# Performance work log

Measured on AMD Instinct MI355X. Metric: run time of the kernel, lower is better.

Reference implementation:

```python
import jax, jax.numpy as jnp
import numpy as np

N_NODES = 10000
N_EDGES = 320000
D_IN = 256
D_OUT = 256
NEG_SLOPE = 0.2


def setup_inputs() -> dict:
    key = jax.random.key(0)
    ks = jax.random.split(key, 8)
    feature = jax.random.normal(ks[0], (N_NODES, D_IN), dtype=jnp.float32)
    src = jax.random.randint(ks[1], (N_EDGES,), 0, N_NODES, dtype=jnp.int32)
    dst = jax.random.randint(ks[2], (N_EDGES,), 0, N_NODES, dtype=jnp.int32)
    # Xavier-ish scaled weights
    s = 1.0 / np.sqrt(D_IN)
    W_s = jax.random.normal(ks[3], (D_OUT, D_IN), dtype=jnp.float32) * s
    W_t = jax.random.normal(ks[4], (D_OUT, D_IN), dtype=jnp.float32) * s
    W_attn = jax.random.normal(ks[5], (1, D_OUT), dtype=jnp.float32) * (1.0 / np.sqrt(D_OUT))
    W_fc = jax.random.normal(ks[6], (D_OUT, D_IN), dtype=jnp.float32) * s
    b_fc = jnp.zeros((D_OUT,), dtype=jnp.float32)
    return {"feature": feature, "src": src, "dst": dst,
            "W_s": W_s, "W_t": W_t, "W_attn": W_attn,
            "W_fc": W_fc, "b_fc": b_fc}


def reference(feature, src, dst, W_s, W_t, W_attn, W_fc, b_fc):
    n = feature.shape[0]
    # Project at node level, then gather (same math as projecting gathered feats).
    proj_s = feature @ W_s.T          # [N, D_OUT]
    proj_t = feature @ W_t.T          # [N, D_OUT]
    # Edge attention logits: attn(LeakyReLU(h_dst + h_src))
    z = proj_s[src] + proj_t[dst]     # [E, D_OUT]
    z = jnp.where(z >= 0, z, NEG_SLOPE * z)
    e = (z @ W_attn.T)[:, 0]          # [E]
    # edge_softmax with norm_by='src': softmax over outgoing edges of each src node
    m = jax.ops.segment_max(e, src, num_segments=n)          # [N]
    m = jnp.where(jnp.isfinite(m), m, 0.0)                   # guard empty segments
    e_exp = jnp.exp(e - m[src])                               # [E]
    denom = jax.ops.segment_sum(e_exp, src, num_segments=n)  # [N]
    alpha = e_exp / denom[src]                                # [E]
    # message = src feature * alpha; reduce = sum at dst
    msg = feature[src] * alpha[:, None]                       # [E, D_IN]
    agg = jax.ops.segment_sum(msg, dst, num_segments=n)       # [N, D_IN]
    # final linear
    return agg @ W_fc.T + b_fc
```

## Files before the change

kernel.cpp:

```cpp
#include <hip/hip_runtime.h>
#include <math.h>

#define N_NODES 10000
#define N_EDGES 320000
#define D 256
#define NEG_SLOPE 0.2f
#define BCAP 96
#define BLOCK 256
#define NF4 (N_NODES * D / 4)
#define NW4 (256 * 256 / 4)
#define NTILE_M 157
#define NTILES (NTILE_M * 12)
#define FILL_BLOCKS ((N_EDGES + BLOCK - 1) / BLOCK)

typedef unsigned short ushortT;
typedef __attribute__((ext_vector_type(8))) short bf16x8;
typedef __attribute__((ext_vector_type(4))) float f32x4;

__device__ __forceinline__ unsigned short f2bf(float f) {
  unsigned int u = __float_as_uint(f);
  u += 0x7FFFu + ((u >> 16) & 1u);
  return (unsigned short)(u >> 16);
}
__device__ __forceinline__ float bf2f(unsigned short u) {
  return __uint_as_float((unsigned int)u << 16);
}

__global__ void prep_kernel(const float* __restrict__ feat,
                            const float* __restrict__ Ws,
                            const float* __restrict__ Wt,
                            const float* __restrict__ Wfc,
                            ushortT* __restrict__ featb,
                            ushortT* __restrict__ Wcat,
                            int* __restrict__ cnt,
                            float* __restrict__ denom) {
  const int g = blockIdx.x * blockDim.x + threadIdx.x;
  if (g < NF4) {
    float4 v = ((const float4*)feat)[g];
    ushort4 u;
    u.x = f2bf(v.x); u.y = f2bf(v.y); u.z = f2bf(v.z); u.w = f2bf(v.w);
    ((ushort4*)featb)[g] = u;
    return;
  }
  const int gi = g - NF4;
  if (gi < 3 * NW4) {
    const float* W = (gi < NW4) ? Ws : ((gi < 2 * NW4) ? Wt : Wfc);
    const int off = gi - ((gi < NW4) ? 0 : ((gi < 2 * NW4) ? NW4 : 2 * NW4));
    float4 v = ((const float4*)W)[off];
    ushort4 u;
    u.x = f2bf(v.x); u.y = f2bf(v.y); u.z = f2bf(v.z); u.w = f2bf(v.w);
    ((ushort4*)Wcat)[gi] = u;
    return;
  }
  const int gn = gi - 3 * NW4;
  if (gn < N_NODES) {
    cnt[gn] = 0;
    denom[gn] = 0.f;
  }
}

__global__ __launch_bounds__(256, 2) void proj_fill_kernel(
    const ushortT* __restrict__ featb,
    const ushortT* __restrict__ Wcat,
    const int* __restrict__ src, const int* __restrict__ dst,
    int* __restrict__ cnt, int* __restrict__ src_b,
    ushortT* __restrict__ ps, ushortT* __restrict__ pt,
    ushortT* __restrict__ fcp) {
  if (blockIdx.x >= NTILES) {
    const int i = (blockIdx.x - NTILES) * BLOCK + threadIdx.x;
    if (i < N_EDGES) {
      const int dn = dst[i];
      const int slot = atomicAdd(&cnt[dn], 1);
      if (slot < BCAP) src_b[dn * BCAP + slot] = src[i];
    }
    return;
  }

  const int m0 = (blockIdx.x % NTILE_M) * 64;
  const int by = blockIdx.x / NTILE_M;
  ushortT* outp = (by < 4) ? ps : ((by < 8) ? pt : fcp);
  const int col0 = (by & 3) * 64;
  const int n0 = by * 64;

  const int wave = threadIdx.x >> 6;
  const int lane = threadIdx.x & 63;
  const int quad = lane >> 4;
  const int l16 = lane & 15;

  const int m_base = m0 + (wave & 1) * 32;
  const int wn = wave >> 1;
  const int nb = n0 + wn * 32;

  const bf16x8 zero8 = {0, 0, 0, 0, 0, 0, 0, 0};
  const int r0 = m_base + l16;
  const int r1 = r0 + 16;

  bf16x8 a0r[8], a1r[8];
#pragma unroll
  for (int kk = 0; kk < 8; ++kk) {
    const int ko = kk * 32 + quad * 8;
    a0r[kk] = (r0 < N_NODES) ? *(const bf16x8*)(featb + (size_t)r0 * D + ko) : zero8;
    a1r[kk] = (r1 < N_NODES) ? *(const bf16x8*)(featb + (size_t)r1 * D + ko) : zero8;
  }

  f32x4 acc[2][2];
#pragma unroll
  for (int i = 0; i < 2; ++i)
#pragma unroll
    for (int j = 0; j < 2; ++j) acc[i][j] = (f32x4){0.f, 0.f, 0.f, 0.f};

#pragma unroll
  for (int kk = 0; kk < 8; ++kk) {
    const int ko = kk * 32 + quad * 8;
    bf16x8 b0 = *(const bf16x8*)(Wcat + (size_t)(nb + l16) * D + ko);
    bf16x8 b1 = *(const bf16x8*)(Wcat + (size_t)(nb + 16 + l16) * D + ko);
    acc[0][0] = __builtin_amdgcn_mfma_f32_16x16x32_bf16(a0r[kk], b0, acc[0][0], 0, 0, 0);
    acc[0][1] = __builtin_amdgcn_mfma_f32_16x16x32_bf16(a0r[kk], b1, acc[0][1], 0, 0, 0);
    acc[1][0] = __builtin_amdgcn_mfma_f32_16x16x32_bf16(a1r[kk], b0, acc[1][0], 0, 0, 0);
    acc[1][1] = __builtin_amdgcn_mfma_f32_16x16x32_bf16(a1r[kk], b1, acc[1][1], 0, 0, 0);
  }

#pragma unroll
  for (int mi = 0; mi < 2; ++mi) {
#pragma unroll
    for (int r = 0; r < 4; ++r) {
      const int row = m_base + mi * 16 + quad * 4 + r;
      if (row < N_NODES) {
#pragma unroll
        for (int ni = 0; ni < 2; ++ni) {
          const int col = col0 + wn * 32 + ni * 16 + l16;
          outp[(size_t)row * D + col] = f2bf(acc[mi][ni][r]);
        }
      }
    }
  }
}

__global__ __launch_bounds__(256) void logit_bucket_kernel(
    const ushortT* __restrict__ ps,
    const ushortT* __restrict__ pt,
    const int* __restrict__ cnt,
    const int* __restrict__ src_b,
    const float* __restrict__ Wattn,
    float* __restrict__ expv_b,
    float* __restrict__ denom) {
  const int n = blockIdx.x;
  const int cn = min(cnt[n], BCAP);
  if (cn == 0) return;
  const int wave = threadIdx.x >> 6;
  const int lane = threadIdx.x & 63;
  const int half = lane >> 5;
  const int l32 = lane & 31;
  const int grp = wave * 2 + half;
  const int base = n * BCAP;

  bf16x8 bu = *(const bf16x8*)(pt + (size_t)n * D + l32 * 8);
  float b[8], w[8];
  const float4 w0 = *(const float4*)(Wattn + l32 * 8);
  const float4 w1 = *(const float4*)(Wattn + l32 * 8 + 4);
  w[0] = w0.x; w[1] = w0.y; w[2] = w0.z; w[3] = w0.w;
  w[4] = w1.x; w[5] = w1.y; w[6] = w1.z; w[7] = w1.w;
#pragma unroll
  for (int i = 0; i < 8; ++i) b[i] = bf2f((unsigned short)bu[i]);

  int j = grp;
  for (; j + 24 < cn; j += 32) {
    const int s0 = src_b[base + j];
    const int s1 = src_b[base + j + 8];
    const int s2 = src_b[base + j + 16];
    const int s3 = src_b[base + j + 24];
    bf16x8 au0 = *(const bf16x8*)(ps + (size_t)s0 * D + l32 * 8);
    bf16x8 au1 = *(const bf16x8*)(ps + (size_t)s1 * D + l32 * 8);
    bf16x8 au2 = *(const bf16x8*)(ps + (size_t)s2 * D + l32 * 8);
    bf16x8 au3 = *(const bf16x8*)(ps + (size_t)s3 * D + l32 * 8);
    float sum0 = 0.f, sum1 = 0.f, sum2 = 0.f, sum3 = 0.f;
#pragma unroll
    for (int i = 0; i < 8; ++i) {
      float z0 = bf2f((unsigned short)au0[i]) + b[i];
      float z1 = bf2f((unsigned short)au1[i]) + b[i];
      float z2 = bf2f((unsigned short)au2[i]) + b[i];
      float z3 = bf2f((unsigned short)au3[i]) + b[i];
      z0 = fmaxf(z0, NEG_SLOPE * z0);
      z1 = fmaxf(z1, NEG_SLOPE * z1);
      z2 = fmaxf(z2, NEG_SLOPE * z2);
      z3 = fmaxf(z3, NEG_SLOPE * z3);
      sum0 = fmaf(w[i], z0, sum0);
      sum1 = fmaf(w[i], z1, sum1);
      sum2 = fmaf(w[i], z2, sum2);
      sum3 = fmaf(w[i], z3, sum3);
    }
#pragma unroll
    for (int off = 16; off > 0; off >>= 1) {
      sum0 += __shfl_down(sum0, off, 32);
      sum1 += __shfl_down(sum1, off, 32);
      sum2 += __shfl_down(sum2, off, 32);
      sum3 += __shfl_down(sum3, off, 32);
    }
    if (l32 == 0) {
      float ex0 = __expf(sum0), ex1 = __expf(sum1);
      float ex2 = __expf(sum2), ex3 = __expf(sum3);
      expv_b[base + j] = ex0;
      expv_b[base + j + 8] = ex1;
      expv_b[base + j + 16] = ex2;
      expv_b[base + j + 24] = ex3;
      atomicAdd(&denom[s0], ex0);
      atomicAdd(&denom[s1], ex1);
      atomicAdd(&denom[s2], ex2);
      atomicAdd(&denom[s3], ex3);
    }
  }
  for (; j < cn; j += 8) {
    const int s = src_b[base + j];
    bf16x8 au = *(const bf16x8*)(ps + (size_t)s * D + l32 * 8);
    float sum = 0.f;
#pragma unroll
    for (int i = 0; i < 8; ++i) {
      float z = bf2f((unsigned short)au[i]) + b[i];
      z = fmaxf(z, NEG_SLOPE * z);
      sum = fmaf(w[i], z, sum);
    }
#pragma unroll
    for (int off = 16; off > 0; off >>= 1) sum += __shfl_down(sum, off, 32);
    if (l32 == 0) {
      float ex = __expf(sum);
      expv_b[base + j] = ex;
      atomicAdd(&denom[s], ex);
    }
  }
}

__global__ __launch_bounds__(64) void prescale_kernel(
    const ushortT* __restrict__ fcp,
    const float* __restrict__ denom,
    ushortT* __restrict__ fcpsb) {
  const int n = blockIdx.x;
  const int t = threadIdx.x;
  const float inv = 1.0f / denom[n];
  ushort4 v = ((const ushort4*)(fcp + (size_t)n * D))[t];
  ushort4 o;
  o.x = f2bf(bf2f(v.x) * inv);
  o.y = f2bf(bf2f(v.y) * inv);
  o.z = f2bf(bf2f(v.z) * inv);
  o.w = f2bf(bf2f(v.w) * inv);
  ((ushort4*)(fcpsb + (size_t)n * D))[t] = o;
}

__global__ __launch_bounds__(256) void gather_agg_kernel(
    const ushortT* __restrict__ fcpsb,
    const int* __restrict__ cnt,
    const int* __restrict__ src_b,
    const float* __restrict__ expv_b,
    const float* __restrict__ b_fc,
    float* __restrict__ out) {
  __shared__ float red[8][D];
  const int n = blockIdx.x;
  const int tid = threadIdx.x;
  const int wave = tid >> 6;
  const int lane = tid & 63;
  const int half = lane >> 5;
  const int l32 = lane & 31;
  const int grp = wave * 2 + half;
  const int cn = min(cnt[n], BCAP);
  const int base = n * BCAP;

  float acc[8];
#pragma unroll
  for (int i = 0; i < 8; ++i) acc[i] = 0.f;

  int j = grp;
  for (; j + 24 < cn; j += 32) {
    const int s0 = src_b[base + j];
    const int s1 = src_b[base + j + 8];
    const int s2 = src_b[base + j + 16];
    const int s3 = src_b[base + j + 24];
    const float a0 = expv_b[base + j];
    const float a1 = expv_b[base + j + 8];
    const float a2 = expv_b[base + j + 16];
    const float a3 = expv_b[base + j + 24];
    bf16x8 f0 = *(const bf16x8*)(fcpsb + (size_t)s0 * D + l32 * 8);
    bf16x8 f1 = *(const bf16x8*)(fcpsb + (size_t)s1 * D + l32 * 8);
    bf16x8 f2 = *(const bf16x8*)(fcpsb + (size_t)s2 * D + l32 * 8);
    bf16x8 f3 = *(const bf16x8*)(fcpsb + (size_t)s3 * D + l32 * 8);
#pragma unroll
    for (int i = 0; i < 8; ++i) {
      acc[i] = fmaf(a0, bf2f((unsigned short)f0[i]), acc[i]);
      acc[i] = fmaf(a1, bf2f((unsigned short)f1[i]), acc[i]);
      acc[i] = fmaf(a2, bf2f((unsigned short)f2[i]), acc[i]);
      acc[i] = fmaf(a3, bf2f((unsigned short)f3[i]), acc[i]);
    }
  }
  for (; j < cn; j += 8) {
    const int s = src_b[base + j];
    const float a = expv_b[base + j];
    bf16x8 fu = *(const bf16x8*)(fcpsb + (size_t)s * D + l32 * 8);
#pragma unroll
    for (int i = 0; i < 8; ++i)
      acc[i] = fmaf(a, bf2f((unsigned short)fu[i]), acc[i]);
  }
  *(float4*)&red[grp][l32 * 8] = make_float4(acc[0], acc[1], acc[2], acc[3]);
  *(float4*)&red[grp][l32 * 8 + 4] = make_float4(acc[4], acc[5], acc[6], acc[7]);
  __syncthreads();
  float o = b_fc[tid];
#pragma unroll
  for (int g = 0; g < 8; ++g) o += red[g][tid];
  out[(size_t)n * D + tid] = o;
}

extern "C" void kernel_launch(void* const* d_in, const int* in_sizes, int n_in,
                              void* d_out, int out_size, void* d_ws, size_t ws_size,
                              hipStream_t stream) {
  const float* feat  = (const float*)d_in[0];
  const int*   src   = (const int*)d_in[1];
  const int*   dst   = (const int*)d_in[2];
  const float* Ws    = (const float*)d_in[3];
  const float* Wt    = (const float*)d_in[4];
  const float* Wattn = (const float*)d_in[5];
  const float* Wfc   = (const float*)d_in[6];
  const float* bfc   = (const float*)d_in[7];
  float* out = (float*)d_out;

  ushortT* ps    = (ushortT*)d_ws;
  ushortT* pt    = ps + (size_t)N_NODES * D;
  ushortT* fcp   = pt + (size_t)N_NODES * D;
  ushortT* featb = fcp + (size_t)N_NODES * D;
  ushortT* Wcat  = featb + (size_t)N_NODES * D;
  float* expv_b  = (float*)(Wcat + (size_t)768 * 256);
  float* denom   = expv_b + (size_t)N_NODES * BCAP;
  int*   cnt     = (int*)(denom + N_NODES);
  int*   src_b   = cnt + N_NODES;
  ushortT* fcpsb = featb;

  const int prep_items = NF4 + 3 * NW4 + N_NODES;
  prep_kernel<<<(prep_items + BLOCK - 1) / BLOCK, BLOCK, 0, stream>>>(
      feat, Ws, Wt, Wfc, featb, Wcat, cnt, denom);
  proj_fill_kernel<<<NTILES + FILL_BLOCKS, BLOCK, 0, stream>>>(
      featb, Wcat, src, dst, cnt, src_b, ps, pt, fcp);
  logit_bucket_kernel<<<N_NODES, BLOCK, 0, stream>>>(ps, pt, cnt, src_b, Wattn, expv_b, denom);
  prescale_kernel<<<N_NODES, 64, 0, stream>>>(fcp, denom, fcpsb);
  gather_agg_kernel<<<N_NODES, BLOCK, 0, stream>>>(fcpsb, cnt, src_b, expv_b, bfc, out);
}
```

Baseline: 179.2 us.

## Stage feature tile in LDS, preload weights, reorder fill blocks first

The projection GEMM now loads each 64-row feature tile cooperatively into padded shared memory, with each wave reading its A fragments from LDS and holding the B weight fragments in registers. Tile blocks are ordered so the 12 column tiles for the same rows run next to each other, improving L2 reuse of the feature rows. Edge-fill blocks are moved to the front of the grid, and launch bounds are raised to allow more resident blocks. The cost is added LDS traffic and a block barrier, and the higher occupancy target may put pressure on registers.

```diff
diff --git a/kernel.cpp b/kernel.cpp
--- a/kernel.cpp
+++ b/kernel.cpp
@@ -12,6 +12,7 @@
 #define NTILE_M 157
 #define NTILES (NTILE_M * 12)
 #define FILL_BLOCKS ((N_EDGES + BLOCK - 1) / BLOCK)
+#define APAD 264
 
 typedef unsigned short ushortT;
 typedef __attribute__((ext_vector_type(8))) short bf16x8;
@@ -59,15 +60,17 @@
   }
 }
 
-__global__ __launch_bounds__(256, 2) void proj_fill_kernel(
+__global__ __launch_bounds__(256, 4) void proj_fill_kernel(
     const ushortT* __restrict__ featb,
     const ushortT* __restrict__ Wcat,
     const int* __restrict__ src, const int* __restrict__ dst,
     int* __restrict__ cnt, int* __restrict__ src_b,
     ushortT* __restrict__ ps, ushortT* __restrict__ pt,
     ushortT* __restrict__ fcp) {
-  if (blockIdx.x >= NTILES) {
-    const int i = (blockIdx.x - NTILES) * BLOCK + threadIdx.x;
+  __shared__ ushortT Als[64][APAD];
+
+  if (blockIdx.x < FILL_BLOCKS) {
+    const int i = blockIdx.x * BLOCK + threadIdx.x;
     if (i < N_EDGES) {
       const int dn = dst[i];
       const int slot = atomicAdd(&cnt[dn], 1);
@@ -75,33 +78,42 @@
     }
     return;
   }
-
-  const int m0 = (blockIdx.x % NTILE_M) * 64;
-  const int by = blockIdx.x / NTILE_M;
+  const int p = blockIdx.x - FILL_BLOCKS;
+  const int m0 = (p / 12) * 64;
+  const int by = p % 12;
   ushortT* outp = (by < 4) ? ps : ((by < 8) ? pt : fcp);
   const int col0 = (by & 3) * 64;
   const int n0 = by * 64;
 
-  const int wave = threadIdx.x >> 6;
-  const int lane = threadIdx.x & 63;
+  const int tid = threadIdx.x;
+  const int wave = tid >> 6;
+  const int lane = tid & 63;
   const int quad = lane >> 4;
   const int l16 = lane & 15;
 
-  const int m_base = m0 + (wave & 1) * 32;
+  const int m_base_t = (wave & 1) * 32;
   const int wn = wave >> 1;
   const int nb = n0 + wn * 32;
 
-  const bf16x8 zero8 = {0, 0, 0, 0, 0, 0, 0, 0};
-  const int r0 = m_base + l16;
-  const int r1 = r0 + 16;
-
-  bf16x8 a0r[8], a1r[8];
+  bf16x8 b0r[8], b1r[8];
 #pragma unroll
   for (int kk = 0; kk < 8; ++kk) {
     const int ko = kk * 32 + quad * 8;
-    a0r[kk] = (r0 < N_NODES) ? *(const bf16x8*)(featb + (size_t)r0 * D + ko) : zero8;
-    a1r[kk] = (r1 < N_NODES) ? *(const bf16x8*)(featb + (size_t)r1 * D + ko) : zero8;
-  }
+    b0r[kk] = *(const bf16x8*)(Wcat + (size_t)(nb + l16) * D + ko);
+    b1r[kk] = *(const bf16x8*)(Wcat + (size_t)(nb + 16 + l16) * D + ko);
+  }
+
+  const int tr = tid >> 2;
+  const int tk = (tid & 3) * 64;
+  const int gr = m0 + tr;
+  const bf16x8 zero8 = {0, 0, 0, 0, 0, 0, 0, 0};
+#pragma unroll
+  for (int i = 0; i < 8; ++i) {
+    bf16x8 av = (gr < N_NODES) ? *(const bf16x8*)(featb + (size_t)gr * D + tk + 8 * i) : zero8;
+    *(bf16x8*)&Als[tr][tk + 8 * i] = av;
+  }
+  __builtin_amdgcn_sched_barrier(0);
+  __syncthreads();
 
   f32x4 acc[2][2];
 #pragma unroll
@@ -109,22 +121,23 @@
 #pragma unroll
     for (int j = 0; j < 2; ++j) acc[i][j] = (f32x4){0.f, 0.f, 0.f, 0.f};
 
+  const int ar0 = m_base_t + l16;
 #pragma unroll
   for (int kk = 0; kk < 8; ++kk) {
     const int ko = kk * 32 + quad * 8;
-    bf16x8 b0 = *(const bf16x8*)(Wcat + (size_t)(nb + l16) * D + ko);
-    bf16x8 b1 = *(const bf16x8*)(Wcat + (size_t)(nb + 16 + l16) * D + ko);
-    acc[0][0] = __builtin_amdgcn_mfma_f32_16x16x32_bf16(a0r[kk], b0, acc[0][0], 0, 0, 0);
-    acc[0][1] = __builtin_amdgcn_mfma_f32_16x16x32_bf16(a0r[kk], b1, acc[0][1], 0, 0, 0);
-    acc[1][0] = __builtin_amdgcn_mfma_f32_16x16x32_bf16(a1r[kk], b0, acc[1][0], 0, 0, 0);
-    acc[1][1] = __builtin_amdgcn_mfma_f32_16x16x32_bf16(a1r[kk], b1, acc[1][1], 0, 0, 0);
+    bf16x8 a0 = *(const bf16x8*)&Als[ar0][ko];
+    bf16x8 a1 = *(const bf16x8*)&Als[ar0 + 16][ko];
+    acc[0][0] = __builtin_amdgcn_mfma_f32_16x16x32_bf16(a0, b0r[kk], acc[0][0], 0, 0, 0);
+    acc[0][1] = __builtin_amdgcn_mfma_f32_16x16x32_bf16(a0, b1r[kk], acc[0][1], 0, 0, 0);
+    acc[1][0] = __builtin_amdgcn_mfma_f32_16x16x32_bf16(a1, b0r[kk], acc[1][0], 0, 0, 0);
+    acc[1][1] = __builtin_amdgcn_mfma_f32_16x16x32_bf16(a1, b1r[kk], acc[1][1], 0, 0, 0);
   }
 
 #pragma unroll
   for (int mi = 0; mi < 2; ++mi) {
 #pragma unroll
     for (int r = 0; r < 4; ++r) {
-      const int row = m_base + mi * 16 + quad * 4 + r;
+      const int row = m0 + m_base_t + mi * 16 + quad * 4 + r;
       if (row < N_NODES) {
 #pragma unroll
         for (int ni = 0; ni < 2; ++ni) {
@@ -333,7 +346,7 @@
   const int prep_items = NF4 + 3 * NW4 + N_NODES;
   prep_kernel<<<(prep_items + BLOCK - 1) / BLOCK, BLOCK, 0, stream>>>(
       feat, Ws, Wt, Wfc, featb, Wcat, cnt, denom);
-  proj_fill_kernel<<<NTILES + FILL_BLOCKS, BLOCK, 0, stream>>>(
+  proj_fill_kernel<<<FILL_BLOCKS + NTILES, BLOCK, 0, stream>>>(
       featb, Wcat, src, dst, cnt, src_b, ps, pt, fcp);
   logit_bucket_kernel<<<N_NODES, BLOCK, 0, stream>>>(ps, pt, cnt, src_b, Wattn, expv_b, denom);
   prescale_kernel<<<N_NODES, 64, 0, stream>>>(fcp, denom, fcpsb);
```

New measurement: 178.6 us. About the same (-0.3%).
